# Kernel tuning notes

Measured on AMD Instinct MI355X. Metric: run time of the kernel, lower is better.

Reference implementation:

```python
import jax, jax.numpy as jnp
import numpy as np

E, D, DIM, H, DH, MLP = 8, 6, 512, 8, 64, 512
P, S, NC, B = 4, 32, 10, 128
PD = 3 * P * P          # patch_dim = 48
GRID = S // P           # 8
N = GRID * GRID + 1     # 65 tokens (64 patches + cls)


def setup_inputs() -> dict:
    key = jax.random.key(0)
    ks = iter(jax.random.split(key, 16))
    r = lambda *s: jax.random.normal(next(ks), s, jnp.float32) * 0.02
    z = lambda *s: jnp.zeros(s, jnp.float32)
    o = lambda *s: jnp.ones(s, jnp.float32)
    return dict(
        x=jax.random.normal(next(ks), (B, 3, S, S), jnp.float32),
        gate_w=r(E, 3 * S * S), gate_b=z(E),
        pln1_g=o(E, PD), pln1_b=z(E, PD),
        patch_w=r(E, PD, DIM), patch_b=z(E, DIM),
        pln2_g=o(E, DIM), pln2_b=z(E, DIM),
        cls_tok=r(E, DIM), pos_emb=r(E, N, DIM),
        aln_g=o(E, D, DIM), aln_b=z(E, D, DIM),
        qkv_w=r(E, D, DIM, 3 * H * DH),
        out_w=r(E, D, H * DH, DIM), out_b=z(E, D, DIM),
        fln_g=o(E, D, DIM), fln_b=z(E, D, DIM),
        ff1_w=r(E, D, DIM, MLP), ff1_b=z(E, D, MLP),
        ff2_w=r(E, D, MLP, DIM), ff2_b=z(E, D, DIM),
        final_g=o(E, DIM), final_b=z(E, DIM),
        head_w=r(E, DIM, NC), head_b=z(E, NC))


def _ln(x, g, b):
    m = x.mean(-1, keepdims=True)
    v = ((x - m) ** 2).mean(-1, keepdims=True)
    return (x - m) * jax.lax.rsqrt(v + 1e-5) * g + b


LAYER_KEYS = ('aln_g', 'aln_b', 'qkv_w', 'out_w', 'out_b',
              'fln_g', 'fln_b', 'ff1_w', 'ff1_b', 'ff2_w', 'ff2_b')


def _vit(x, p):
    # x: [B, 3, S, S]; p: per-expert param dict (no leading expert axis)
    Bx = x.shape[0]
    # rearrange 'b c (h p1) (w p2) -> b (h w) (p1 p2 c)'
    t = x.reshape(Bx, 3, GRID, P, GRID, P).transpose(0, 2, 4, 3, 5, 1)
    t = t.reshape(Bx, GRID * GRID, PD)
    t = _ln(t, p['pln1_g'], p['pln1_b'])
    t = t @ p['patch_w'] + p['patch_b']
    t = _ln(t, p['pln2_g'], p['pln2_b'])
    cls = jnp.broadcast_to(p['cls_tok'][None, None, :], (Bx, 1, DIM))
    t = jnp.concatenate([cls, t], axis=1) + p['pos_emb'][None]  # [B, N, DIM]

    def block(t, lp):
        g = _ln(t, lp['aln_g'], lp['aln_b'])
        qkv = g @ lp['qkv_w']                       # [B, N, 3*H*DH]
        q, k, v = jnp.split(qkv, 3, axis=-1)
        q = q.reshape(Bx, N, H, DH).transpose(0, 2, 1, 3)
        k = k.reshape(Bx, N, H, DH).transpose(0, 2, 1, 3)
        v = v.reshape(Bx, N, H, DH).transpose(0, 2, 1, 3)
        att = jax.nn.softmax(jnp.einsum('bhid,bhjd->bhij', q, k) * (DH ** -0.5), axis=-1)
        o = jnp.einsum('bhij,bhjd->bhid', att, v).transpose(0, 2, 1, 3).reshape(Bx, N, H * DH)
        t = t + o @ lp['out_w'] + lp['out_b']
        g = _ln(t, lp['fln_g'], lp['fln_b'])
        f = jax.nn.gelu(g @ lp['ff1_w'] + lp['ff1_b'], approximate=False) @ lp['ff2_w'] + lp['ff2_b']
        return t + f, None

    layer_p = {k: p[k] for k in LAYER_KEYS}  # each [D, ...]
    t, _ = jax.lax.scan(block, t, layer_p)
    t = _ln(t, p['final_g'], p['final_b'])
    return t[:, 0] @ p['head_w'] + p['head_b']   # [B, NC]


def _moe(x, params):
    Bx = x.shape[0]
    logits = x.reshape(Bx, -1) @ params['gate_w'].T + params['gate_b']  # [B, E]
    top1 = jnp.argmax(logits, axis=1)                                   # [B]
    expert_p = {k: v for k, v in params.items() if k not in ('gate_w', 'gate_b')}
    all_out = jax.vmap(lambda pp: _vit(x, pp))(expert_p)                # [E, B, NC]
    return all_out[top1, jnp.arange(Bx)]                                # [B, NC]


def reference(x, gate_w, gate_b, pln1_g, pln1_b, patch_w, patch_b, pln2_g, pln2_b,
              cls_tok, pos_emb, aln_g, aln_b, qkv_w, out_w, out_b,
              fln_g, fln_b, ff1_w, ff1_b, ff2_w, ff2_b, final_g, final_b,
              head_w, head_b):
    params = {k: v for k, v in locals().items() if k != 'x'}
    return _moe(x, params)
```

## Files before the change

### kernel.cpp

```cpp
#include <hip/hip_runtime.h>
#include <math.h>

#define EXPERTS 8
#define DEPTH 6
#define DIM 512
#define HEADS 8
#define NCLS 10
#define BATCH 128
#define PD 48
#define NTOK 65
#define NRT 73
#define NROWSP (NRT * 128)

typedef __attribute__((ext_vector_type(4))) float f32x4;
typedef __attribute__((ext_vector_type(8))) __bf16 bf16x8;
typedef unsigned short u16;

#define GLOAD_LDS16(gp, lp)                                                     \
    __builtin_amdgcn_global_load_lds(                                           \
        (const __attribute__((address_space(1))) void*)(gp),                    \
        (__attribute__((address_space(3))) void*)(lp), 16, 0, 0)

__device__ inline u16 f2bf(float f) {
    union { float f; unsigned u; } v; v.f = f;
    unsigned r = v.u + 0x7FFFu + ((v.u >> 16) & 1u);
    return (u16)(r >> 16);
}
__device__ inline float bf2f(u16 s) {
    union { unsigned u; float f; } v; v.u = ((unsigned)s) << 16;
    return v.f;
}

__global__ __launch_bounds__(256) void gate_k(const float* __restrict__ x,
                                              const float* __restrict__ gw,
                                              const float* __restrict__ gb,
                                              int* __restrict__ top1) {
    int b = blockIdx.x, tid = threadIdx.x;
    const float* xb = x + (size_t)b * 3072;
    float acc[EXPERTS];
#pragma unroll
    for (int e = 0; e < EXPERTS; ++e) acc[e] = 0.f;
    for (int i = tid; i < 3072; i += 256) {
        float xv = xb[i];
#pragma unroll
        for (int e = 0; e < EXPERTS; ++e)
            acc[e] = fmaf(xv, gw[(size_t)e * 3072 + i], acc[e]);
    }
    __shared__ float red[256];
    __shared__ float logits[EXPERTS];
    for (int e = 0; e < EXPERTS; ++e) {
        red[tid] = acc[e];
        __syncthreads();
        for (int s = 128; s > 0; s >>= 1) {
            if (tid < s) red[tid] += red[tid + s];
            __syncthreads();
        }
        if (tid == 0) logits[e] = red[0] + gb[e];
        __syncthreads();
    }
    if (tid == 0) {
        int best = 0;
        float bv = logits[0];
        for (int e = 1; e < EXPERTS; ++e)
            if (logits[e] > bv) { bv = logits[e]; best = e; }
        top1[b] = best;
    }
}

__global__ __launch_bounds__(128) void route3_k(const int* __restrict__ top1,
                                                int* __restrict__ prow,
                                                int* __restrict__ tile_e) {
    __shared__ int t1[BATCH];
    int tid = threadIdx.x;
    t1[tid] = top1[tid];
    __syncthreads();
    if (tid != 0) return;
    int row = 0, tile = 0;
    for (int e = 0; e < EXPERTS; ++e) {
        int ne = 0;
        for (int b = 0; b < BATCH; ++b)
            if (t1[b] == e) { prow[b] = row + ne * 65; ne++; }
        if (!ne) continue;
        int nt = (ne * 65 + 127) >> 7;
        for (int tt = 0; tt < nt; ++tt) tile_e[tile++] = e;
        row += nt << 7;
    }
    for (; tile < NRT; ++tile) tile_e[tile] = -1;
}

__global__ __launch_bounds__(256) void patch_k(const float* __restrict__ x,
                                               const float* __restrict__ pln1_g,
                                               const float* __restrict__ pln1_b,
                                               const float* __restrict__ patch_w,
                                               const float* __restrict__ patch_b,
                                               const float* __restrict__ pln2_g,
                                               const float* __restrict__ pln2_b,
                                               const float* __restrict__ cls_tok,
                                               const float* __restrict__ pos_emb,
                                               const int* __restrict__ top1,
                                               const int* __restrict__ prow,
                                               float* __restrict__ t) {
    int n = blockIdx.x, b = blockIdx.y, tid = threadIdx.x;
    int e = top1[b];
    float* trow = t + ((size_t)prow[b] + n) * DIM;
    const float* pe = pos_emb + ((size_t)e * NTOK + n) * DIM;

    if (n == 0) {
        for (int d = tid; d < DIM; d += 256)
            trow[d] = cls_tok[e * DIM + d] + pe[d];
        return;
    }
    int pi = n - 1, h = pi >> 3, w = pi & 7;
    __shared__ float pv[PD];
    __shared__ float red[256];
    if (tid < PD) {
        int p1 = tid / 12, rem = tid % 12, p2 = rem / 3, c = rem % 3;
        pv[tid] = x[((size_t)b * 3 + c) * 1024 + (h * 4 + p1) * 32 + (w * 4 + p2)];
    }
    __syncthreads();
    float m = 0.f, q = 0.f;
    for (int j = 0; j < PD; ++j) { float v = pv[j]; m += v; q += v * v; }
    m *= (1.f / PD);
    q = q * (1.f / PD) - m * m;
    float rs = rsqrtf(q + 1e-5f);
    __syncthreads();
    if (tid < PD)
        pv[tid] = (pv[tid] - m) * rs * pln1_g[e * PD + tid] + pln1_b[e * PD + tid];
    __syncthreads();

    float acc0 = patch_b[e * DIM + tid];
    float acc1 = patch_b[e * DIM + tid + 256];
    for (int j = 0; j < PD; ++j) {
        float v = pv[j];
        const float* wr = patch_w + ((size_t)e * PD + j) * DIM;
        acc0 = fmaf(v, wr[tid], acc0);
        acc1 = fmaf(v, wr[tid + 256], acc1);
    }
    red[tid] = acc0 + acc1;
    __syncthreads();
    for (int s = 128; s > 0; s >>= 1) {
        if (tid < s) red[tid] += red[tid + s];
        __syncthreads();
    }
    float S = red[0];
    __syncthreads();
    red[tid] = acc0 * acc0 + acc1 * acc1;
    __syncthreads();
    for (int s = 128; s > 0; s >>= 1) {
        if (tid < s) red[tid] += red[tid + s];
        __syncthreads();
    }
    float Q = red[0];
    float mean = S * (1.f / DIM);
    float var = Q * (1.f / DIM) - mean * mean;
    float rs2 = rsqrtf(var + 1e-5f);
    trow[tid]       = (acc0 - mean) * rs2 * pln2_g[e * DIM + tid]       + pln2_b[e * DIM + tid]       + pe[tid];
    trow[tid + 256] = (acc1 - mean) * rs2 * pln2_g[e * DIM + tid + 256] + pln2_b[e * DIM + tid + 256] + pe[tid + 256];
}

__global__ __launch_bounds__(256) void ln2_k(const float* __restrict__ src,
                                             u16* __restrict__ dst,
                                             const float* __restrict__ gbase,
                                             const float* __restrict__ bbase,
                                             const int* __restrict__ tile_e,
                                             int gestride) {
    int row = blockIdx.x * 4 + (threadIdx.x >> 6);
    int lane = threadIdx.x & 63;
    int e = tile_e[row >> 7];
    if (e < 0) return;
    const float* s = src + (size_t)row * 512;
    float4 a = *(const float4*)&s[lane * 4];
    float4 b = *(const float4*)&s[256 + lane * 4];
    float sum = a.x + a.y + a.z + a.w + b.x + b.y + b.z + b.w;
    float sq = a.x * a.x + a.y * a.y + a.z * a.z + a.w * a.w +
               b.x * b.x + b.y * b.y + b.z * b.z + b.w * b.w;
#pragma unroll
    for (int off = 32; off > 0; off >>= 1) {
        sum += __shfl_xor(sum, off);
        sq += __shfl_xor(sq, off);
    }
    float mean = sum * (1.f / DIM);
    float rs = rsqrtf(sq * (1.f / DIM) - mean * mean + 1e-5f);
    const float* g = gbase + (size_t)e * gestride;
    const float* bb = bbase + (size_t)e * gestride;
    float4 g0 = *(const float4*)&g[lane * 4];
    float4 g1 = *(const float4*)&g[256 + lane * 4];
    float4 b0 = *(const float4*)&bb[lane * 4];
    float4 b1 = *(const float4*)&bb[256 + lane * 4];
    int swz = (row & 7) << 3;
    u16 o[4];
    o[0] = f2bf((a.x - mean) * rs * g0.x + b0.x);
    o[1] = f2bf((a.y - mean) * rs * g0.y + b0.y);
    o[2] = f2bf((a.z - mean) * rs * g0.z + b0.z);
    o[3] = f2bf((a.w - mean) * rs * g0.w + b0.w);
    *(int2*)&dst[(size_t)row * 512 + ((lane * 4) ^ swz)] = *(int2*)o;
    o[0] = f2bf((b.x - mean) * rs * g1.x + b1.x);
    o[1] = f2bf((b.y - mean) * rs * g1.y + b1.y);
    o[2] = f2bf((b.z - mean) * rs * g1.z + b1.z);
    o[3] = f2bf((b.w - mean) * rs * g1.w + b1.w);
    *(int2*)&dst[(size_t)row * 512 + ((256 + lane * 4) ^ swz)] = *(int2*)o;
}

__global__ __launch_bounds__(256) void wconv_k(const float* __restrict__ src,
                                               u16* __restrict__ dst, int N) {
    __shared__ float tile[32][33];
    int n0 = blockIdx.x * 32, k0 = blockIdx.y * 32, m = blockIdx.z;
    const float* s = src + (size_t)m * 512 * N;
    u16* d = dst + (size_t)m * 512 * N;
    int r = threadIdx.x >> 5, c = threadIdx.x & 31;
#pragma unroll
    for (int i = 0; i < 4; ++i)
        tile[r + i * 8][c] = s[(size_t)(k0 + r + i * 8) * N + n0 + c];
    __syncthreads();
#pragma unroll
    for (int i = 0; i < 4; ++i) {
        int n = n0 + r + i * 8;
        d[(size_t)n * 512 + ((k0 + c) ^ ((n & 7) << 3))] = f2bf(tile[c][r + i * 8]);
    }
}

template <int N, int OP>
__global__ __launch_bounds__(256) void mgemm5_k(const u16* __restrict__ A,
                                                const u16* __restrict__ Wtbase,
                                                const float* __restrict__ Bbase,
                                                void* __restrict__ Cptr,
                                                const int* __restrict__ tile_e,
                                                int westride, int bestride) {
    constexpr int CT = N / 128;
    int orig = blockIdx.x, nwg = NRT * CT;
    int q = nwg >> 3, r8 = nwg & 7;
    int xcd = orig & 7, off = orig >> 3;
    int wg = (xcd < r8 ? xcd * (q + 1) : r8 * (q + 1) + (xcd - r8) * q) + off;
    int tile = wg / CT, ct = wg - tile * CT;
    int e = tile_e[tile];
    if (e < 0) return;
    int row0 = tile * 128, c0 = ct * 128;
    const u16* Wt = Wtbase + (size_t)e * westride;

    int tid = threadIdx.x;
    int lane = tid & 63, w = tid >> 6;
    int rl = lane & 15, kg = lane >> 4;
    int wr = w >> 1, wc = w & 1;

    __shared__ __align__(16) u16 As[128 * 64];
    __shared__ __align__(16) u16 Bs[128 * 64];

    f32x4 acc[4][4];
#pragma unroll
    for (int mt = 0; mt < 4; ++mt)
#pragma unroll
        for (int nt = 0; nt < 4; ++nt) acc[mt][nt] = (f32x4){0.f, 0.f, 0.f, 0.f};

    const u16* Ag = A + (size_t)(row0 + w * 32 + (lane >> 3)) * 512 + (lane & 7) * 8;
    const u16* Bg = Wt + (size_t)(c0 + w * 32 + (lane >> 3)) * 512 + (lane & 7) * 8;
    u16* Asw = As + w * 2048;
    u16* Bsw = Bs + w * 2048;

    int blk0 = (kg ^ (rl & 7)) * 8;
    int blk1 = ((4 + kg) ^ (rl & 7)) * 8;

    for (int k0 = 0; k0 < 512; k0 += 64) {
#pragma unroll
        for (int i = 0; i < 4; ++i) {
            GLOAD_LDS16(Ag + k0 + i * 8 * 512, Asw + i * 512);
            GLOAD_LDS16(Bg + k0 + i * 8 * 512, Bsw + i * 512);
        }
        __syncthreads();
#pragma unroll
        for (int ks = 0; ks < 2; ++ks) {
            int blk = ks ? blk1 : blk0;
            bf16x8 av[4], bv[4];
#pragma unroll
            for (int i = 0; i < 4; ++i) {
                av[i] = *(const bf16x8*)&As[(wr * 64 + i * 16 + rl) * 64 + blk];
                bv[i] = *(const bf16x8*)&Bs[(wc * 64 + i * 16 + rl) * 64 + blk];
            }
#pragma unroll
            for (int mt = 0; mt < 4; ++mt)
#pragma unroll
                for (int nt = 0; nt < 4; ++nt)
                    acc[mt][nt] = __builtin_amdgcn_mfma_f32_16x16x32_bf16(
                        av[mt], bv[nt], acc[mt][nt], 0, 0, 0);
        }
        __syncthreads();
    }

    int rh = lane >> 4;
#pragma unroll
    for (int mt = 0; mt < 4; ++mt)
#pragma unroll
        for (int nt = 0; nt < 4; ++nt)
#pragma unroll
            for (int rr = 0; rr < 4; ++rr) {
                size_t grow = row0 + wr * 64 + mt * 16 + rh * 4 + rr;
                int c = c0 + wc * 64 + nt * 16 + rl;
                float v = acc[mt][nt][rr];
                if (OP == 0) {
                    ((u16*)Cptr)[grow * N + c] = f2bf(v);
                } else if (OP == 1) {
                    ((float*)Cptr)[grow * 512 + c] += v + Bbase[(size_t)e * bestride + c];
                } else {
                    float vb = v + Bbase[(size_t)e * bestride + c];
                    float gl = vb * 0.5f * (1.f + erff(vb * 0.70710678118f));
                    ((u16*)Cptr)[grow * 512 + (c ^ (((int)grow & 7) << 3))] = f2bf(gl);
                }
            }
}

#define ATT_LDS (23040 / 2 + 8320 / 2 + 12288 / 2)
__global__ __launch_bounds__(256) void attn2_k(const u16* __restrict__ qkv,
                                               u16* __restrict__ o,
                                               const int* __restrict__ prow) {
    int h = blockIdx.x, b = blockIdx.y, tid = threadIdx.x;
    int pr = prow[b];
    __shared__ __align__(16) u16 smem[ATT_LDS];
    u16* Qs = smem;
    u16* Ks = smem + 80 * 72;
    u16* Ps = smem;
    u16* Vs = smem + 2 * 80 * 72;
    u16* Vt = Vs + 65 * 64;

    const u16* base = qkv + (size_t)pr * 1536 + h * 64;

    for (int idx = tid; idx < 640; idx += 256) {
        int r = idx >> 3, q = idx & 7;
        int4 vq = {0, 0, 0, 0}, vk = {0, 0, 0, 0};
        if (r < NTOK) {
            vq = *(const int4*)&base[(size_t)r * 1536 + q * 8];
            vk = *(const int4*)&base[(size_t)r * 1536 + 512 + q * 8];
        }
        *(int4*)&Qs[r * 72 + q * 8] = vq;
        *(int4*)&Ks[r * 72 + q * 8] = vk;
    }
    for (int idx = tid; idx < 520; idx += 256) {
        int r = idx >> 3, q = idx & 7;
        *(int4*)&Vs[r * 64 + q * 8] = *(const int4*)&base[(size_t)r * 1536 + 1024 + q * 8];
    }
    __syncthreads();

    int lane = tid & 63, w = tid >> 6;
    int rl = lane & 15, kg = lane >> 4, g = lane >> 4;

    f32x4 acc[2][5];
#pragma unroll
    for (int mi = 0; mi < 2; ++mi)
#pragma unroll
        for (int nt = 0; nt < 5; ++nt) acc[mi][nt] = (f32x4){0.f, 0.f, 0.f, 0.f};

#pragma unroll
    for (int mi = 0; mi < 2; ++mi) {
        if (mi == 1 && w != 0) continue;
        int mt = (mi == 0) ? w : 4;
        bf16x8 av0 = *(const bf16x8*)&Qs[(mt * 16 + rl) * 72 + kg * 8];
        bf16x8 av1 = *(const bf16x8*)&Qs[(mt * 16 + rl) * 72 + 32 + kg * 8];
#pragma unroll
        for (int nt = 0; nt < 5; ++nt) {
            bf16x8 bv0 = *(const bf16x8*)&Ks[(nt * 16 + rl) * 72 + kg * 8];
            bf16x8 bv1 = *(const bf16x8*)&Ks[(nt * 16 + rl) * 72 + 32 + kg * 8];
            acc[mi][nt] = __builtin_amdgcn_mfma_f32_16x16x32_bf16(av0, bv0, acc[mi][nt], 0, 0, 0);
            acc[mi][nt] = __builtin_amdgcn_mfma_f32_16x16x32_bf16(av1, bv1, acc[mi][nt], 0, 0, 0);
        }
    }

    for (int idx = tid; idx < 768; idx += 256) {
        int d = idx & 63, kq = idx >> 6;
        u16 tmp[8];
#pragma unroll
        for (int j = 0; j < 8; ++j) {
            int k = kq * 8 + j;
            tmp[j] = (k < NTOK) ? Vs[k * 64 + d] : (u16)0;
        }
        *(int4*)&Vt[d * 96 + kq * 8] = *(int4*)tmp;
    }

#pragma unroll
    for (int mi = 0; mi < 2; ++mi) {
        if (mi == 1 && w != 0) continue;
#pragma unroll
        for (int r = 0; r < 4; ++r) {
            float m = -3.0e38f;
#pragma unroll
            for (int nt = 0; nt < 5; ++nt) {
                float s = acc[mi][nt][r] * 0.125f;
                if (nt * 16 + rl >= NTOK) s = -3.0e38f;
                acc[mi][nt][r] = s;
                m = fmaxf(m, s);
            }
            m = fmaxf(m, __shfl_xor(m, 1));
            m = fmaxf(m, __shfl_xor(m, 2));
            m = fmaxf(m, __shfl_xor(m, 4));
            m = fmaxf(m, __shfl_xor(m, 8));
            float sum = 0.f;
#pragma unroll
            for (int nt = 0; nt < 5; ++nt) {
                float p = expf(acc[mi][nt][r] - m);
                acc[mi][nt][r] = p;
                sum += p;
            }
            sum += __shfl_xor(sum, 1);
            sum += __shfl_xor(sum, 2);
            sum += __shfl_xor(sum, 4);
            sum += __shfl_xor(sum, 8);
            float inv = 1.f / sum;
#pragma unroll
            for (int nt = 0; nt < 5; ++nt) acc[mi][nt][r] *= inv;
        }
    }
    __syncthreads();

#pragma unroll
    for (int mi = 0; mi < 2; ++mi) {
        if (mi == 1 && w != 0) continue;
        int mt = (mi == 0) ? w : 4;
#pragma unroll
        for (int nt = 0; nt < 5; ++nt)
#pragma unroll
            for (int r = 0; r < 4; ++r)
                Ps[(mt * 16 + g * 4 + r) * 96 + nt * 16 + rl] = f2bf(acc[mi][nt][r]);
    }
    for (int idx = tid; idx < 160; idx += 256) {
        int r = idx >> 1, hf = idx & 1;
        *(int4*)&Ps[r * 96 + 80 + hf * 8] = (int4){0, 0, 0, 0};
    }
    __syncthreads();

#pragma unroll
    for (int mi = 0; mi < 2; ++mi) {
        if (mi == 1 && w != 0) continue;
        int mt = (mi == 0) ? w : 4;
#pragma unroll
        for (int dt = 0; dt < 4; ++dt) {
            f32x4 oa = {0.f, 0.f, 0.f, 0.f};
#pragma unroll
            for (int s2 = 0; s2 < 3; ++s2) {
                bf16x8 av = *(const bf16x8*)&Ps[(mt * 16 + rl) * 96 + s2 * 32 + kg * 8];
                bf16x8 bv = *(const bf16x8*)&Vt[(dt * 16 + rl) * 96 + s2 * 32 + kg * 8];
                oa = __builtin_amdgcn_mfma_f32_16x16x32_bf16(av, bv, oa, 0, 0, 0);
            }
#pragma unroll
            for (int r = 0; r < 4; ++r) {
                int row = mt * 16 + g * 4 + r;
                if (row < NTOK) {
                    int grow = pr + row;
                    int c = h * 64 + dt * 16 + rl;
                    o[(size_t)grow * DIM + (c ^ ((grow & 7) << 3))] = f2bf(oa[r]);
                }
            }
        }
    }
}

__global__ __launch_bounds__(64) void final_k(const float* __restrict__ t,
                                              const float* __restrict__ fg,
                                              const float* __restrict__ fb,
                                              const float* __restrict__ hw,
                                              const float* __restrict__ hb,
                                              const int* __restrict__ top1,
                                              const int* __restrict__ prow,
                                              float* __restrict__ out) {
    int b = blockIdx.x, lane = threadIdx.x;
    int e = top1[b];
    const float* row = t + (size_t)prow[b] * DIM;
    float v[8], s = 0.f, q = 0.f;
#pragma unroll
    for (int ii = 0; ii < 8; ++ii) {
        v[ii] = row[ii * 64 + lane];
        s += v[ii];
        q += v[ii] * v[ii];
    }
    for (int off = 32; off > 0; off >>= 1) {
        s += __shfl_xor(s, off);
        q += __shfl_xor(q, off);
    }
    float mean = s * (1.f / DIM);
    float var = q * (1.f / DIM) - mean * mean;
    float rs = rsqrtf(var + 1e-5f);
    float nv[8];
#pragma unroll
    for (int ii = 0; ii < 8; ++ii) {
        int d = ii * 64 + lane;
        nv[ii] = (v[ii] - mean) * rs * fg[e * DIM + d] + fb[e * DIM + d];
    }
    for (int c = 0; c < NCLS; ++c) {
        float p = 0.f;
#pragma unroll
        for (int ii = 0; ii < 8; ++ii) {
            int d = ii * 64 + lane;
            p = fmaf(nv[ii], hw[(size_t)e * DIM * NCLS + d * NCLS + c], p);
        }
        for (int off = 32; off > 0; off >>= 1) p += __shfl_xor(p, off);
        if (lane == 0) out[b * NCLS + c] = p + hb[e * NCLS + c];
    }
}

extern "C" void kernel_launch(void* const* d_in, const int* in_sizes, int n_in,
                              void* d_out, int out_size, void* d_ws, size_t ws_size,
                              hipStream_t stream) {
    const float* x       = (const float*)d_in[0];
    const float* gate_w  = (const float*)d_in[1];
    const float* gate_b  = (const float*)d_in[2];
    const float* pln1_g  = (const float*)d_in[3];
    const float* pln1_b  = (const float*)d_in[4];
    const float* patch_w = (const float*)d_in[5];
    const float* patch_b = (const float*)d_in[6];
    const float* pln2_g  = (const float*)d_in[7];
    const float* pln2_b  = (const float*)d_in[8];
    const float* cls_tok = (const float*)d_in[9];
    const float* pos_emb = (const float*)d_in[10];
    const float* aln_g   = (const float*)d_in[11];
    const float* aln_b   = (const float*)d_in[12];
    const float* qkv_w   = (const float*)d_in[13];
    const float* out_w   = (const float*)d_in[14];
    const float* out_b   = (const float*)d_in[15];
    const float* fln_g   = (const float*)d_in[16];
    const float* fln_b   = (const float*)d_in[17];
    const float* ff1_w   = (const float*)d_in[18];
    const float* ff1_b   = (const float*)d_in[19];
    const float* ff2_w   = (const float*)d_in[20];
    const float* ff2_b   = (const float*)d_in[21];
    const float* final_g = (const float*)d_in[22];
    const float* final_b = (const float*)d_in[23];
    const float* head_w  = (const float*)d_in[24];
    const float* head_b  = (const float*)d_in[25];
    float* out = (float*)d_out;

    int* top1   = (int*)d_ws;
    int* prow   = top1 + 128;
    int* tile_e = prow + 128;
    float* t  = (float*)((char*)d_ws + 4096);
    u16* aln  = (u16*)(t + (size_t)NROWSP * DIM);
    u16* qb16 = aln + (size_t)NROWSP * DIM;
    u16* ao16 = qb16 + (size_t)NROWSP * 1536;
    u16* h16  = ao16 + (size_t)NROWSP * DIM;
    u16* wq_t = h16 + (size_t)NROWSP * DIM;
    u16* wo_t = wq_t + (size_t)48 * 1536 * 512;
    u16* w1_t = wo_t + (size_t)48 * 512 * 512;
    u16* w2_t = w1_t + (size_t)48 * 512 * 512;

    gate_k<<<BATCH, 256, 0, stream>>>(x, gate_w, gate_b, top1);
    route3_k<<<1, 128, 0, stream>>>(top1, prow, tile_e);
    patch_k<<<dim3(NTOK, BATCH), 256, 0, stream>>>(x, pln1_g, pln1_b, patch_w, patch_b,
                                                   pln2_g, pln2_b, cls_tok, pos_emb,
                                                   top1, prow, t);
    wconv_k<<<dim3(48, 16, 48), 256, 0, stream>>>(qkv_w, wq_t, 1536);
    wconv_k<<<dim3(16, 16, 48), 256, 0, stream>>>(out_w, wo_t, 512);
    wconv_k<<<dim3(16, 16, 48), 256, 0, stream>>>(ff1_w, w1_t, 512);
    wconv_k<<<dim3(16, 16, 48), 256, 0, stream>>>(ff2_w, w2_t, 512);

    for (int l = 0; l < DEPTH; ++l) {
        ln2_k<<<NROWSP / 4, 256, 0, stream>>>(t, aln, aln_g + l * DIM, aln_b + l * DIM,
                                              tile_e, DEPTH * DIM);
        mgemm5_k<1536, 0><<<NRT * 12, 256, 0, stream>>>(
            aln, wq_t + (size_t)l * 1536 * 512, nullptr, qb16, tile_e,
            DEPTH * 512 * 1536, 0);
        attn2_k<<<dim3(HEADS, BATCH), 256, 0, stream>>>(qb16, ao16, prow);
        mgemm5_k<512, 1><<<NRT * 4, 256, 0, stream>>>(
            ao16, wo_t + (size_t)l * 512 * 512, out_b + l * DIM, t, tile_e,
            DEPTH * 512 * 512, DEPTH * DIM);
        ln2_k<<<NROWSP / 4, 256, 0, stream>>>(t, aln, fln_g + l * DIM, fln_b + l * DIM,
                                              tile_e, DEPTH * DIM);
        mgemm5_k<512, 2><<<NRT * 4, 256, 0, stream>>>(
            aln, w1_t + (size_t)l * 512 * 512, ff1_b + l * DIM, h16, tile_e,
            DEPTH * 512 * 512, DEPTH * DIM);
        mgemm5_k<512, 1><<<NRT * 4, 256, 0, stream>>>(
            h16, w2_t + (size_t)l * 512 * 512, ff2_b + l * DIM, t, tile_e,
            DEPTH * 512 * 512, DEPTH * DIM);
    }
    final_k<<<BATCH, 64, 0, stream>>>(t, final_g, final_b, head_w, head_b, top1, prow, out);
}
```

Measured before the change: 882.8 us.

## Use 256-row expert tiles with 512-thread QKV GEMM and 5-wave attention

Routing now pads each expert's rows to 256-row tiles, and a new 512-thread QKV GEMM kernel handles 256x128 output tiles so each weight tile loaded into shared memory is reused across twice as many rows. The other GEMMs keep 128-row tiles but look up the expert via tile>>1. Attention now launches 320 threads so each of the 5 waves owns one 16-row query tile, removing the extra serial pass that wave 0 previously did for the fifth tile. Coarser tiles add more padding rows per expert, which means extra wasted compute and more memory for the padded buffers.

```diff
diff --git a/kernel.cpp b/kernel.cpp
--- a/kernel.cpp
+++ b/kernel.cpp
@@ -9,8 +9,9 @@
 #define BATCH 128
 #define PD 48
 #define NTOK 65
-#define NRT 73
-#define NROWSP (NRT * 128)
+#define NRT256 40
+#define NRT128 80
+#define NROWSP (NRT256 * 256)
 
 typedef __attribute__((ext_vector_type(4))) float f32x4;
 typedef __attribute__((ext_vector_type(8))) __bf16 bf16x8;
@@ -81,11 +82,11 @@
         for (int b = 0; b < BATCH; ++b)
             if (t1[b] == e) { prow[b] = row + ne * 65; ne++; }
         if (!ne) continue;
-        int nt = (ne * 65 + 127) >> 7;
+        int nt = (ne * 65 + 255) >> 8;
         for (int tt = 0; tt < nt; ++tt) tile_e[tile++] = e;
-        row += nt << 7;
-    }
-    for (; tile < NRT; ++tile) tile_e[tile] = -1;
+        row += nt << 8;
+    }
+    for (; tile < NRT256; ++tile) tile_e[tile] = -1;
 }
 
 __global__ __launch_bounds__(256) void patch_k(const float* __restrict__ x,
@@ -166,7 +167,7 @@
                                              int gestride) {
     int row = blockIdx.x * 4 + (threadIdx.x >> 6);
     int lane = threadIdx.x & 63;
-    int e = tile_e[row >> 7];
+    int e = tile_e[row >> 8];
     if (e < 0) return;
     const float* s = src + (size_t)row * 512;
     float4 a = *(const float4*)&s[lane * 4];
@@ -219,20 +220,98 @@
     }
 }
 
-template <int N, int OP>
+__global__ __launch_bounds__(512) void mgemm6_k(const u16* __restrict__ A,
+                                                const u16* __restrict__ Wtbase,
+                                                u16* __restrict__ C,
+                                                const int* __restrict__ tile_e,
+                                                int westride) {
+    constexpr int N = 1536, CT = 12;
+    int orig = blockIdx.x, nwg = NRT256 * CT;
+    int q = nwg >> 3, r8 = nwg & 7;
+    int xcd = orig & 7, off = orig >> 3;
+    int wg = (xcd < r8 ? xcd * (q + 1) : r8 * (q + 1) + (xcd - r8) * q) + off;
+    int tile = wg / CT, ct = wg - tile * CT;
+    int e = tile_e[tile];
+    if (e < 0) return;
+    int row0 = tile * 256, c0 = ct * 128;
+    const u16* Wt = Wtbase + (size_t)e * westride;
+
+    int tid = threadIdx.x;
+    int lane = tid & 63, w = tid >> 6;
+    int rl = lane & 15, kg = lane >> 4;
+    int wr = w >> 1, wc = w & 1;
+
+    __shared__ __align__(16) u16 As[256 * 64];
+    __shared__ __align__(16) u16 Bs[128 * 64];
+
+    f32x4 acc[4][4];
+#pragma unroll
+    for (int mt = 0; mt < 4; ++mt)
+#pragma unroll
+        for (int nt = 0; nt < 4; ++nt) acc[mt][nt] = (f32x4){0.f, 0.f, 0.f, 0.f};
+
+    const u16* Ag = A + (size_t)(row0 + w * 32 + (lane >> 3)) * 512 + (lane & 7) * 8;
+    const u16* Bg = Wt + (size_t)(c0 + w * 16 + (lane >> 3)) * 512 + (lane & 7) * 8;
+    u16* Asw = As + w * 2048;
+    u16* Bsw = Bs + w * 1024;
+
+    int blk0 = (kg ^ (rl & 7)) * 8;
+    int blk1 = ((4 + kg) ^ (rl & 7)) * 8;
+
+    for (int k0 = 0; k0 < 512; k0 += 64) {
+#pragma unroll
+        for (int i = 0; i < 4; ++i)
+            GLOAD_LDS16(Ag + k0 + i * 8 * 512, Asw + i * 512);
+#pragma unroll
+        for (int i = 0; i < 2; ++i)
+            GLOAD_LDS16(Bg + k0 + i * 8 * 512, Bsw + i * 512);
+        __syncthreads();
+#pragma unroll
+        for (int ks = 0; ks < 2; ++ks) {
+            int blk = ks ? blk1 : blk0;
+            bf16x8 av[4], bv[4];
+#pragma unroll
+            for (int i = 0; i < 4; ++i) {
+                av[i] = *(const bf16x8*)&As[(wr * 64 + i * 16 + rl) * 64 + blk];
+                bv[i] = *(const bf16x8*)&Bs[(wc * 64 + i * 16 + rl) * 64 + blk];
+            }
+#pragma unroll
+            for (int mt = 0; mt < 4; ++mt)
+#pragma unroll
+                for (int nt = 0; nt < 4; ++nt)
+                    acc[mt][nt] = __builtin_amdgcn_mfma_f32_16x16x32_bf16(
+                        av[mt], bv[nt], acc[mt][nt], 0, 0, 0);
+        }
+        __syncthreads();
+    }
+
+    int rh = lane >> 4;
+#pragma unroll
+    for (int mt = 0; mt < 4; ++mt)
+#pragma unroll
+        for (int nt = 0; nt < 4; ++nt)
+#pragma unroll
+            for (int rr = 0; rr < 4; ++rr) {
+                size_t grow = row0 + wr * 64 + mt * 16 + rh * 4 + rr;
+                int c = c0 + wc * 64 + nt * 16 + rl;
+                C[grow * N + c] = f2bf(acc[mt][nt][rr]);
+            }
+}
+
+template <int OP>
 __global__ __launch_bounds__(256) void mgemm5_k(const u16* __restrict__ A,
                                                 const u16* __restrict__ Wtbase,
                                                 const float* __restrict__ Bbase,
                                                 void* __restrict__ Cptr,
                                                 const int* __restrict__ tile_e,
                                                 int westride, int bestride) {
-    constexpr int CT = N / 128;
-    int orig = blockIdx.x, nwg = NRT * CT;
+    constexpr int CT = 4;
+    int orig = blockIdx.x, nwg = NRT128 * CT;
     int q = nwg >> 3, r8 = nwg & 7;
     int xcd = orig & 7, off = orig >> 3;
     int wg = (xcd < r8 ? xcd * (q + 1) : r8 * (q + 1) + (xcd - r8) * q) + off;
     int tile = wg / CT, ct = wg - tile * CT;
-    int e = tile_e[tile];
+    int e = tile_e[tile >> 1];
     if (e < 0) return;
     int row0 = tile * 128, c0 = ct * 128;
     const u16* Wt = Wtbase + (size_t)e * westride;
@@ -295,9 +374,7 @@
                 size_t grow = row0 + wr * 64 + mt * 16 + rh * 4 + rr;
                 int c = c0 + wc * 64 + nt * 16 + rl;
                 float v = acc[mt][nt][rr];
-                if (OP == 0) {
-                    ((u16*)Cptr)[grow * N + c] = f2bf(v);
-                } else if (OP == 1) {
+                if (OP == 1) {
                     ((float*)Cptr)[grow * 512 + c] += v + Bbase[(size_t)e * bestride + c];
                 } else {
                     float vb = v + Bbase[(size_t)e * bestride + c];
@@ -308,7 +385,7 @@
 }
 
 #define ATT_LDS (23040 / 2 + 8320 / 2 + 12288 / 2)
-__global__ __launch_bounds__(256) void attn2_k(const u16* __restrict__ qkv,
+__global__ __launch_bounds__(320) void attn3_k(const u16* __restrict__ qkv,
                                                u16* __restrict__ o,
                                                const int* __restrict__ prow) {
     int h = blockIdx.x, b = blockIdx.y, tid = threadIdx.x;
@@ -322,7 +399,7 @@
 
     const u16* base = qkv + (size_t)pr * 1536 + h * 64;
 
-    for (int idx = tid; idx < 640; idx += 256) {
+    for (int idx = tid; idx < 640; idx += 320) {
         int r = idx >> 3, q = idx & 7;
         int4 vq = {0, 0, 0, 0}, vk = {0, 0, 0, 0};
         if (r < NTOK) {
@@ -332,37 +409,32 @@
         *(int4*)&Qs[r * 72 + q * 8] = vq;
         *(int4*)&Ks[r * 72 + q * 8] = vk;
     }
-    for (int idx = tid; idx < 520; idx += 256) {
+    for (int idx = tid; idx < 520; idx += 320) {
         int r = idx >> 3, q = idx & 7;
         *(int4*)&Vs[r * 64 + q * 8] = *(const int4*)&base[(size_t)r * 1536 + 1024 + q * 8];
     }
     __syncthreads();
 
-    int lane = tid & 63, w = tid >> 6;
+    int lane = tid & 63, mt = tid >> 6;
     int rl = lane & 15, kg = lane >> 4, g = lane >> 4;
 
-    f32x4 acc[2][5];
-#pragma unroll
-    for (int mi = 0; mi < 2; ++mi)
-#pragma unroll
-        for (int nt = 0; nt < 5; ++nt) acc[mi][nt] = (f32x4){0.f, 0.f, 0.f, 0.f};
-
-#pragma unroll
-    for (int mi = 0; mi < 2; ++mi) {
-        if (mi == 1 && w != 0) continue;
-        int mt = (mi == 0) ? w : 4;
+    f32x4 acc[5];
+#pragma unroll
+    for (int nt = 0; nt < 5; ++nt) acc[nt] = (f32x4){0.f, 0.f, 0.f, 0.f};
+
+    {
         bf16x8 av0 = *(const bf16x8*)&Qs[(mt * 16 + rl) * 72 + kg * 8];
         bf16x8 av1 = *(const bf16x8*)&Qs[(mt * 16 + rl) * 72 + 32 + kg * 8];
 #pragma unroll
         for (int nt = 0; nt < 5; ++nt) {
             bf16x8 bv0 = *(const bf16x8*)&Ks[(nt * 16 + rl) * 72 + kg * 8];
             bf16x8 bv1 = *(const bf16x8*)&Ks[(nt * 16 + rl) * 72 + 32 + kg * 8];
-            acc[mi][nt] = __builtin_amdgcn_mfma_f32_16x16x32_bf16(av0, bv0, acc[mi][nt], 0, 0, 0);
-            acc[mi][nt] = __builtin_amdgcn_mfma_f32_16x16x32_bf16(av1, bv1, acc[mi][nt], 0, 0, 0);
-        }
-    }
-
-    for (int idx = tid; idx < 768; idx += 256) {
+            acc[nt] = __builtin_amdgcn_mfma_f32_16x16x32_bf16(av0, bv0, acc[nt], 0, 0, 0);
+            acc[nt] = __builtin_amdgcn_mfma_f32_16x16x32_bf16(av1, bv1, acc[nt], 0, 0, 0);
+        }
+    }
+
+    for (int idx = tid; idx < 768; idx += 320) {
         int d = idx & 63, kq = idx >> 6;
         u16 tmp[8];
 #pragma unroll
@@ -374,77 +446,63 @@
     }
 
 #pragma unroll
-    for (int mi = 0; mi < 2; ++mi) {
-        if (mi == 1 && w != 0) continue;
-#pragma unroll
-        for (int r = 0; r < 4; ++r) {
-            float m = -3.0e38f;
-#pragma unroll
-            for (int nt = 0; nt < 5; ++nt) {
-                float s = acc[mi][nt][r] * 0.125f;
-                if (nt * 16 + rl >= NTOK) s = -3.0e38f;
-                acc[mi][nt][r] = s;
-                m = fmaxf(m, s);
-            }
-            m = fmaxf(m, __shfl_xor(m, 1));
-            m = fmaxf(m, __shfl_xor(m, 2));
-            m = fmaxf(m, __shfl_xor(m, 4));
-            m = fmaxf(m, __shfl_xor(m, 8));
-            float sum = 0.f;
-#pragma unroll
-            for (int nt = 0; nt < 5; ++nt) {
-                float p = expf(acc[mi][nt][r] - m);
-                acc[mi][nt][r] = p;
-                sum += p;
-            }
-            sum += __shfl_xor(sum, 1);
-            sum += __shfl_xor(sum, 2);
-            sum += __shfl_xor(sum, 4);
-            sum += __shfl_xor(sum, 8);
-            float inv = 1.f / sum;
-#pragma unroll
-            for (int nt = 0; nt < 5; ++nt) acc[mi][nt][r] *= inv;
-        }
-    }
-    __syncthreads();
-
-#pragma unroll
-    for (int mi = 0; mi < 2; ++mi) {
-        if (mi == 1 && w != 0) continue;
-        int mt = (mi == 0) ? w : 4;
-#pragma unroll
-        for (int nt = 0; nt < 5; ++nt)
-#pragma unroll
-            for (int r = 0; r < 4; ++r)
-                Ps[(mt * 16 + g * 4 + r) * 96 + nt * 16 + rl] = f2bf(acc[mi][nt][r]);
-    }
-    for (int idx = tid; idx < 160; idx += 256) {
+    for (int r = 0; r < 4; ++r) {
+        float m = -3.0e38f;
+#pragma unroll
+        for (int nt = 0; nt < 5; ++nt) {
+            float s = acc[nt][r] * 0.125f;
+            if (nt * 16 + rl >= NTOK) s = -3.0e38f;
+            acc[nt][r] = s;
+            m = fmaxf(m, s);
+        }
+        m = fmaxf(m, __shfl_xor(m, 1));
+        m = fmaxf(m, __shfl_xor(m, 2));
+        m = fmaxf(m, __shfl_xor(m, 4));
+        m = fmaxf(m, __shfl_xor(m, 8));
+        float sum = 0.f;
+#pragma unroll
+        for (int nt = 0; nt < 5; ++nt) {
+            float p = expf(acc[nt][r] - m);
+            acc[nt][r] = p;
+            sum += p;
+        }
+        sum += __shfl_xor(sum, 1);
+        sum += __shfl_xor(sum, 2);
+        sum += __shfl_xor(sum, 4);
+        sum += __shfl_xor(sum, 8);
+        float inv = 1.f / sum;
+#pragma unroll
+        for (int nt = 0; nt < 5; ++nt) acc[nt][r] *= inv;
+    }
+    __syncthreads();
+
+#pragma unroll
+    for (int nt = 0; nt < 5; ++nt)
+#pragma unroll
+        for (int r = 0; r < 4; ++r)
+            Ps[(mt * 16 + g * 4 + r) * 96 + nt * 16 + rl] = f2bf(acc[nt][r]);
+    for (int idx = tid; idx < 160; idx += 320) {
         int r = idx >> 1, hf = idx & 1;
         *(int4*)&Ps[r * 96 + 80 + hf * 8] = (int4){0, 0, 0, 0};
     }
     __syncthreads();
 
 #pragma unroll
-    for (int mi = 0; mi < 2; ++mi) {
-        if (mi == 1 && w != 0) continue;
-        int mt = (mi == 0) ? w : 4;
-#pragma unroll
-        for (int dt = 0; dt < 4; ++dt) {
-            f32x4 oa = {0.f, 0.f, 0.f, 0.f};
-#pragma unroll
-            for (int s2 = 0; s2 < 3; ++s2) {
-                bf16x8 av = *(const bf16x8*)&Ps[(mt * 16 + rl) * 96 + s2 * 32 + kg * 8];
-                bf16x8 bv = *(const bf16x8*)&Vt[(dt * 16 + rl) * 96 + s2 * 32 + kg * 8];
-                oa = __builtin_amdgcn_mfma_f32_16x16x32_bf16(av, bv, oa, 0, 0, 0);
-            }
-#pragma unroll
-            for (int r = 0; r < 4; ++r) {
-                int row = mt * 16 + g * 4 + r;
-                if (row < NTOK) {
-                    int grow = pr + row;
-                    int c = h * 64 + dt * 16 + rl;
-                    o[(size_t)grow * DIM + (c ^ ((grow & 7) << 3))] = f2bf(oa[r]);
-                }
+    for (int dt = 0; dt < 4; ++dt) {
+        f32x4 oa = {0.f, 0.f, 0.f, 0.f};
+#pragma unroll
+        for (int s2 = 0; s2 < 3; ++s2) {
+            bf16x8 av = *(const bf16x8*)&Ps[(mt * 16 + rl) * 96 + s2 * 32 + kg * 8];
+            bf16x8 bv = *(const bf16x8*)&Vt[(dt * 16 + rl) * 96 + s2 * 32 + kg * 8];
+            oa = __builtin_amdgcn_mfma_f32_16x16x32_bf16(av, bv, oa, 0, 0, 0);
+        }
+#pragma unroll
+        for (int r = 0; r < 4; ++r) {
+            int row = mt * 16 + g * 4 + r;
+            if (row < NTOK) {
+                int grow = pr + row;
+                int c = h * 64 + dt * 16 + rl;
+                o[(size_t)grow * DIM + (c ^ ((grow & 7) << 3))] = f2bf(oa[r]);
             }
         }
     }
@@ -550,19 +608,18 @@
     for (int l = 0; l < DEPTH; ++l) {
         ln2_k<<<NROWSP / 4, 256, 0, stream>>>(t, aln, aln_g + l * DIM, aln_b + l * DIM,
                                               tile_e, DEPTH * DIM);
-        mgemm5_k<1536, 0><<<NRT * 12, 256, 0, stream>>>(
-            aln, wq_t + (size_t)l * 1536 * 512, nullptr, qb16, tile_e,
-            DEPTH * 512 * 1536, 0);
-        attn2_k<<<dim3(HEADS, BATCH), 256, 0, stream>>>(qb16, ao16, prow);
-        mgemm5_k<512, 1><<<NRT * 4, 256, 0, stream>>>(
+        mgemm6_k<<<NRT256 * 12, 512, 0, stream>>>(
+            aln, wq_t + (size_t)l * 1536 * 512, qb16, tile_e, DEPTH * 512 * 1536);
+        attn3_k<<<dim3(HEADS, BATCH), 320, 0, stream>>>(qb16, ao16, prow);
+        mgemm5_k<1><<<NRT128 * 4, 256, 0, stream>>>(
             ao16, wo_t + (size_t)l * 512 * 512, out_b + l * DIM, t, tile_e,
             DEPTH * 512 * 512, DEPTH * DIM);
         ln2_k<<<NROWSP / 4, 256, 0, stream>>>(t, aln, fln_g + l * DIM, fln_b + l * DIM,
                                               tile_e, DEPTH * DIM);
-        mgemm5_k<512, 2><<<NRT * 4, 256, 0, stream>>>(
+        mgemm5_k<2><<<NRT128 * 4, 256, 0, stream>>>(
             aln, w1_t + (size_t)l * 512 * 512, ff1_b + l * DIM, h16, tile_e,
             DEPTH * 512 * 512, DEPTH * DIM);
-        mgemm5_k<512, 1><<<NRT * 4, 256, 0, stream>>>(
+        mgemm5_k<1><<<NRT128 * 4, 256, 0, stream>>>(
             h16, w2_t + (size_t)l * 512 * 512, ff2_b + l * DIM, t, tile_e,
             DEPTH * 512 * 512, DEPTH * DIM);
     }
```

Measured after the change: 863.3 us. 2.2% less time.
